# Kernel optimization log

Hardware: AMD Instinct MI355X
Metric: run time of the kernel (lower is better)

## Reference

```python
import jax, jax.numpy as jnp
import numpy as np

B, C, HW, S, G = 256, 512, 16, 256, 32
EPS = 1e-5


def setup_inputs() -> dict:
    key = jax.random.key(0)
    ks = jax.random.split(key, 6)
    scale = 0.02
    return {
        "x": jax.random.normal(ks[0], (B, C, HW, HW), dtype=jnp.float32),
        "gn_w": jnp.ones((C,), dtype=jnp.float32),
        "gn_b": jnp.zeros((C,), dtype=jnp.float32),
        "wq": jax.random.normal(ks[1], (C, C), dtype=jnp.float32) * scale,
        "bq": jnp.zeros((C,), dtype=jnp.float32),
        "wk": jax.random.normal(ks[2], (C, C), dtype=jnp.float32) * scale,
        "bk": jnp.zeros((C,), dtype=jnp.float32),
        "wv": jax.random.normal(ks[3], (C, C), dtype=jnp.float32) * scale,
        "bv": jnp.zeros((C,), dtype=jnp.float32),
        "wp": jax.random.normal(ks[4], (C, C), dtype=jnp.float32) * scale,
        "bp": jnp.zeros((C,), dtype=jnp.float32),
    }


def reference(x, gn_w, gn_b, wq, bq, wk, bk, wv, bv, wp, bp):
    b = x.shape[0]
    # GroupNorm(32, 512): normalize over (channels-in-group, H, W)
    xg = x.reshape(b, G, C // G, HW, HW)
    mu = jnp.mean(xg, axis=(2, 3, 4), keepdims=True)
    var = jnp.var(xg, axis=(2, 3, 4), keepdims=True)
    h = ((xg - mu) * jax.lax.rsqrt(var + EPS)).reshape(b, C, HW, HW)
    h = h * gn_w[:, None, None] + gn_b[:, None, None]
    hf = h.reshape(b, C, S)  # [B, C, S] with S = H*W = 256
    # 1x1 convs == per-pixel linear projections
    q = jnp.einsum('oc,bcs->bos', wq, hf) + bq[:, None]
    k = jnp.einsum('oc,bcs->bos', wk, hf) + bk[:, None]
    v = jnp.einsum('oc,bcs->bos', wv, hf) + bv[:, None]
    # w[b,s,t] = sum_c q[b,c,s] k[b,c,t]; scaled by sqrt(C)=sqrt(512) per source
    att = jnp.einsum('bcs,bct->bst', q, k) / jnp.sqrt(jnp.float32(C))
    att = jax.nn.softmax(att, axis=2)
    # torch: bmm(v, att.permute(0,2,1)) -> out[b,c,t] = sum_s v[b,c,s] att[b,t,s]
    o = jnp.einsum('bcs,bts->bct', v, att)
    o = o.reshape(b, C, HW, HW)
    o = jnp.einsum('oc,bchw->bohw', wp, o) + bp[None, :, None, None]
    return x + o
```

## Files before the change

### kernel.cpp

```cpp
#include <hip/hip_runtime.h>

typedef __attribute__((ext_vector_type(8))) short short8;
typedef __attribute__((ext_vector_type(8))) unsigned short us8;
typedef __attribute__((ext_vector_type(4))) unsigned short us4;
typedef __attribute__((ext_vector_type(4))) float f32x4;

static __device__ __forceinline__ unsigned short f2bf(float f) {
  union { float f; unsigned u; } c; c.f = f;
  unsigned r = (c.u + 0x7FFFu + ((c.u >> 16) & 1u)) >> 16;
  return (unsigned short)r;
}
static __device__ __forceinline__ float b2f(unsigned short h) {
  union { unsigned u; float f; } c; c.u = ((unsigned)h) << 16; return c.f;
}

static __device__ __forceinline__ void gll16(const unsigned short* g, unsigned short* l) {
  __builtin_amdgcn_global_load_lds(
      (const __attribute__((address_space(1))) unsigned int*)g,
      (__attribute__((address_space(3))) unsigned int*)l, 16, 0, 0);
}

__global__ __launch_bounds__(256) void conv_k(
    const float* __restrict__ wv, const float* __restrict__ wp,
    unsigned short* __restrict__ wvb, unsigned short* __restrict__ wpb)
{
  int i4 = (blockIdx.x * 256 + threadIdx.x) * 4;
  const float* src;
  unsigned short* dst;
  if (i4 < 262144) { src = wv + i4; dst = wvb + i4; }
  else             { src = wp + (i4 - 262144); dst = wpb + (i4 - 262144); }
  f32x4 v = *(const f32x4*)src;
  us4 o;
  #pragma unroll
  for (int j = 0; j < 4; ++j) o[j] = f2bf(v[j]);
  *(us4*)dst = o;
}

__global__ __launch_bounds__(256) void tk(
    const float* __restrict__ wq, const float* __restrict__ wk,
    unsigned short* __restrict__ wqT, unsigned short* __restrict__ wkT)
{
  __shared__ float L[64][65];
  const float* src = blockIdx.z ? wk : wq;
  unsigned short* dst = blockIdx.z ? wkT : wqT;
  const int ro = blockIdx.x * 64, co = blockIdx.y * 64;
  const int tid = threadIdx.x;
  #pragma unroll
  for (int p = 0; p < 4; ++p) {
    int lin = p * 1024 + tid * 4;
    int r = lin >> 6, cl = lin & 63;
    *(f32x4*)&L[r][cl] = *(const f32x4*)(src + (size_t)(ro + r) * 512 + co + cl);
  }
  __syncthreads();
  #pragma unroll
  for (int p = 0; p < 4; ++p) {
    int lin = p * 1024 + tid * 4;
    int rr = lin >> 6, cc = lin & 63;
    us4 o;
    #pragma unroll
    for (int j = 0; j < 4; ++j) o[j] = f2bf(L[cc + j][rr]);
    *(us4*)(dst + (size_t)(co + rr) * 512 + ro + cc) = o;
  }
}

__global__ __launch_bounds__(256) void w2b_k(
    const unsigned short* __restrict__ wkT, const float* __restrict__ bq,
    float* __restrict__ w2b)
{
  const int wv_ = threadIdx.x >> 6, lane = threadIdx.x & 63;
  for (int i = 0; i < 16; ++i) {
    const int c = blockIdx.x * 64 + i * 4 + wv_;
    us8 kv = *(const us8*)(wkT + (size_t)c * 512 + lane * 8);
    float s = 0.f;
    #pragma unroll
    for (int j = 0; j < 8; ++j) s += b2f(kv[j]) * bq[lane * 8 + j];
    #pragma unroll
    for (int o = 32; o; o >>= 1) s += __shfl_xor(s, o);
    if (lane == 0) w2b[c] = s;
  }
}

__global__ __launch_bounds__(512) void gn_k(
    const float* __restrict__ x, const float* __restrict__ gw,
    const float* __restrict__ gb, unsigned short* __restrict__ hT)
{
  __shared__ unsigned short tile[32][256];
  __shared__ float rs[2][4][2];
  const int b = blockIdx.x >> 4, gp = blockIdx.x & 15;
  const int tid = threadIdx.x;
  const int sub = tid >> 8;
  const int t = tid & 255;
  const int g = gp * 2 + sub;
  const float* xp = x + ((size_t)b * 512 + g * 16) * 256;
  f32x4 vals[4];
  float s = 0.f, s2 = 0.f;
  #pragma unroll
  for (int j = 0; j < 4; ++j) {
    f32x4 v = *(const f32x4*)(xp + j * 1024 + t * 4);
    vals[j] = v;
    s  += v[0] + v[1] + v[2] + v[3];
    s2 += v[0]*v[0] + v[1]*v[1] + v[2]*v[2] + v[3]*v[3];
  }
  #pragma unroll
  for (int o = 32; o; o >>= 1) { s += __shfl_xor(s, o); s2 += __shfl_xor(s2, o); }
  if ((t & 63) == 0) { rs[sub][t >> 6][0] = s; rs[sub][t >> 6][1] = s2; }
  __syncthreads();
  s  = rs[sub][0][0] + rs[sub][1][0] + rs[sub][2][0] + rs[sub][3][0];
  s2 = rs[sub][0][1] + rs[sub][1][1] + rs[sub][2][1] + rs[sub][3][1];
  const float mean = s * (1.f / 4096.f);
  const float var  = s2 * (1.f / 4096.f) - mean * mean;
  const float rstd = rsqrtf(var + 1e-5f);
  #pragma unroll
  for (int j = 0; j < 4; ++j) {
    const int cl = j * 4 + (t >> 6);
    const int c = g * 16 + cl;
    const float sc = gw[c] * rstd;
    const float sh = gb[c] - mean * sc;
    f32x4 v = vals[j];
    us4 o;
    #pragma unroll
    for (int q = 0; q < 4; ++q) o[q] = f2bf(v[q] * sc + sh);
    *(us4*)&tile[sub * 16 + cl][(t & 63) * 4] = o;
  }
  __syncthreads();
  const int srow = tid >> 1, half = tid & 1;
  us8 o0, o1;
  #pragma unroll
  for (int c = 0; c < 8; ++c) o0[c] = tile[half * 16 + c][srow];
  #pragma unroll
  for (int c = 0; c < 8; ++c) o1[c] = tile[half * 16 + 8 + c][srow];
  unsigned short* dst = hT + ((size_t)b * 256 + srow) * 512 + gp * 32 + half * 16;
  *(us8*)dst = o0;
  *(us8*)(dst + 8) = o1;
}

template<int BM, int BN, int MI, int TPB, int NWN, int NTT,
         int BIAS_MODE, bool OUT_F32, bool HAS_RESID, bool NFAST, int SWZ = 0>
__global__ __launch_bounds__(TPB, 2) void gemmp_k(
    const unsigned short* __restrict__ A, long long sAb, int lda,
    const unsigned short* __restrict__ B, long long sBb, int ldb,
    void* __restrict__ Cv, long long sCb, int ldc,
    const float* __restrict__ bias, const float* __restrict__ resid)
{
  constexpr int CA = BM * 8 / TPB;
  constexpr int CB = BN * 8 / TPB;
  __shared__ unsigned short SMEM[2 * BM * 64 + 2 * BN * 64];
  unsigned short* AsBase = SMEM;
  unsigned short* BsBase = SMEM + 2 * BM * 64;
  const int tid = threadIdx.x;
  int bz, bm, bn;
  if (SWZ) {
    const int L = blockIdx.x;
    const int xcd = L & 7, j = (L >> 3) & 7, bhi = L >> 6;
    bz = bhi * 8 + xcd;
    bm = (j >> 1) * BM;
    bn = (j & 1) * BN;
  } else {
    bz = blockIdx.z;
    bm = (NFAST ? blockIdx.y : blockIdx.x) * BM;
    bn = (NFAST ? blockIdx.x : blockIdx.y) * BN;
  }
  const int lane = tid & 63, w = tid >> 6;
  const int wr = w / NWN, wc = w % NWN;
  const int lr = lane & 15, lg = lane >> 4;
  const int csw = lr & 7;
  const int ko0 = (lg ^ csw) * 8;
  const int ko1 = ((4 + lg) ^ csw) * 8;

  const unsigned short* aSrc[CA]; int aOff[CA];
  #pragma unroll
  for (int p = 0; p < CA; ++p) {
    const int id = p * TPB + tid;
    const int row = id >> 3, cc = (id & 7) ^ (row & 7);
    aSrc[p] = A + (size_t)bz * sAb + (size_t)(bm + row) * lda + cc * 8;
    aOff[p] = id * 8;
  }
  const unsigned short* bSrc[CB]; int bOff[CB];
  #pragma unroll
  for (int p = 0; p < CB; ++p) {
    const int id = p * TPB + tid;
    const int row = id >> 3, cc = (id & 7) ^ (row & 7);
    bSrc[p] = B + (size_t)bz * sBb + (size_t)(bn + row) * ldb + cc * 8;
    bOff[p] = id * 8;
  }

  f32x4 acc[MI][4];
  #pragma unroll
  for (int i = 0; i < MI; ++i)
    #pragma unroll
    for (int j = 0; j < 4; ++j) acc[i][j] = (f32x4){0.f, 0.f, 0.f, 0.f};

  #pragma unroll
  for (int p = 0; p < CA; ++p) gll16(aSrc[p], &AsBase[aOff[p]]);
  #pragma unroll
  for (int p = 0; p < CB; ++p) gll16(bSrc[p], &BsBase[bOff[p]]);
  asm volatile("s_waitcnt vmcnt(0)" ::: "memory");
  __builtin_amdgcn_s_barrier();

  #pragma unroll 2
  for (int t = 0; t < NTT; ++t) {
    if (t + 1 < NTT) {
      const int k1 = (t + 1) * 64, sl = (t + 1) & 1;
      #pragma unroll
      for (int p = 0; p < CA; ++p) gll16(aSrc[p] + k1, &AsBase[sl * BM * 64 + aOff[p]]);
      #pragma unroll
      for (int p = 0; p < CB; ++p) gll16(bSrc[p] + k1, &BsBase[sl * BN * 64 + bOff[p]]);
    }
    const unsigned short* At = &AsBase[(t & 1) * BM * 64];
    const unsigned short* Bt = &BsBase[(t & 1) * BN * 64];
    short8 bf[4][2];
    #pragma unroll
    for (int nj = 0; nj < 4; ++nj) {
      bf[nj][0] = *(const short8*)(Bt + (wc * 64 + nj * 16 + lr) * 64 + ko0);
      bf[nj][1] = *(const short8*)(Bt + (wc * 64 + nj * 16 + lr) * 64 + ko1);
    }
    #pragma unroll
    for (int h = 0; h < MI / 4; ++h) {
      short8 af[4][2];
      #pragma unroll
      for (int mi = 0; mi < 4; ++mi) {
        const int rr = wr * (MI * 16) + h * 64 + mi * 16 + lr;
        af[mi][0] = *(const short8*)(At + rr * 64 + ko0);
        af[mi][1] = *(const short8*)(At + rr * 64 + ko1);
      }
      __builtin_amdgcn_s_setprio(1);
      #pragma unroll
      for (int mi = 0; mi < 4; ++mi)
        #pragma unroll
        for (int nj = 0; nj < 4; ++nj) {
          acc[h * 4 + mi][nj] = __builtin_amdgcn_mfma_f32_16x16x32_bf16(af[mi][0], bf[nj][0], acc[h * 4 + mi][nj], 0, 0, 0);
          acc[h * 4 + mi][nj] = __builtin_amdgcn_mfma_f32_16x16x32_bf16(af[mi][1], bf[nj][1], acc[h * 4 + mi][nj], 0, 0, 0);
        }
      __builtin_amdgcn_s_setprio(0);
    }
    if (t + 1 < NTT) {
      asm volatile("s_waitcnt vmcnt(0)" ::: "memory");
      __builtin_amdgcn_s_barrier();
    }
  }

  #pragma unroll
  for (int mi = 0; mi < MI; ++mi) {
    #pragma unroll
    for (int r = 0; r < 4; ++r) {
      const int rowc = bm + wr * (MI * 16) + mi * 16 + lg * 4 + r;
      const float bv_ = (BIAS_MODE == 1) ? bias[rowc] : 0.f;
      #pragma unroll
      for (int ni = 0; ni < 4; ++ni) {
        const int col = bn + wc * 64 + ni * 16 + lr;
        float vv = acc[mi][ni][r] + bv_;
        if (BIAS_MODE == 2) vv += bias[col];
        const size_t idx = (size_t)bz * sCb + (size_t)rowc * ldc + col;
        if (HAS_RESID) vv += resid[idx];
        if (OUT_F32) ((float*)Cv)[idx] = vv;
        else ((unsigned short*)Cv)[idx] = f2bf(vv);
      }
    }
  }
}

__global__ __launch_bounds__(512, 1) void fused_k(
    const unsigned short* __restrict__ A,
    const unsigned short* __restrict__ B,
    const unsigned short* __restrict__ V,
    unsigned short* __restrict__ O)
{
  __shared__ __attribute__((aligned(16))) char SM[147456];
  unsigned short* AsB = (unsigned short*)SM;
  unsigned short* BsB = (unsigned short*)(SM + 65536);
  unsigned short* attL = (unsigned short*)SM;
  unsigned short* vbuf = (unsigned short*)(SM + 131072);
  float* redm = (float*)(SM + 131072);
  float* reds = redm + 1024;

  const int tid = threadIdx.x;
  const int bz = blockIdx.z;
  const int lane = tid & 63, w = tid >> 6;
  const int wr = w >> 2, wc = w & 3;
  const int lr = lane & 15, lg = lane >> 4;
  const int csw = lr & 7;
  const int ko0 = (lg ^ csw) * 8;
  const int ko1 = ((4 + lg) ^ csw) * 8;

  const int rl = tid >> 3;
  const int gc = (tid & 7) ^ (rl & 7);
  const unsigned short* pA = A + (size_t)bz * 131072 + (size_t)rl * 512 + gc * 8;
  const unsigned short* pB = B + (size_t)bz * 131072 + (size_t)rl * 512 + gc * 8;

  auto stageA = [&](int t, int h) {
    const unsigned short* s = pA + (size_t)h * 65536 + t * 64;
    unsigned short* d = AsB + ((2 * t + h) & 3) * 8192 + tid * 8;
    gll16(s, d);
    gll16(s + 32768, d + 4096);
  };
  auto stageB = [&](int t, int h) {
    const unsigned short* s = pB + (size_t)h * 65536 + t * 64;
    unsigned short* d = BsB + ((2 * t + h) & 3) * 8192 + tid * 8;
    gll16(s, d);
    gll16(s + 32768, d + 4096);
  };

  f32x4 acc[8][4];
  #pragma unroll
  for (int i = 0; i < 8; ++i)
    #pragma unroll
    for (int j = 0; j < 4; ++j) acc[i][j] = (f32x4){0.f, 0.f, 0.f, 0.f};

  stageA(0, 0); stageA(0, 1); stageB(0, 0); stageB(0, 1);
  stageB(1, 0); stageA(1, 0); stageA(1, 1);
  asm volatile("s_waitcnt vmcnt(6)" ::: "memory");
  __builtin_amdgcn_s_barrier();

  constexpr int NT = 8;
  for (int t = 0; t < NT; ++t) {
    const unsigned short* sA = AsB + ((2 * t + wr) & 3) * 8192;
    const unsigned short* sB = BsB + ((2 * t + (wc >> 1)) & 3) * 8192;
    const int bc = (wc & 1) * 64;
    short8 af[4][2], bf0[2][2], bf1[2][2];

    #pragma unroll
    for (int mi = 0; mi < 4; ++mi) {
      af[mi][0] = *(const short8*)(sA + (mi * 16 + lr) * 64 + ko0);
      af[mi][1] = *(const short8*)(sA + (mi * 16 + lr) * 64 + ko1);
    }
    #pragma unroll
    for (int nj = 0; nj < 2; ++nj) {
      bf0[nj][0] = *(const short8*)(sB + (bc + nj * 16 + lr) * 64 + ko0);
      bf0[nj][1] = *(const short8*)(sB + (bc + nj * 16 + lr) * 64 + ko1);
    }
    if (t + 1 < NT) stageB(t + 1, 1);
    __builtin_amdgcn_s_barrier();
    __builtin_amdgcn_s_setprio(1);
    #pragma unroll
    for (int mi = 0; mi < 4; ++mi)
      #pragma unroll
      for (int nj = 0; nj < 2; ++nj) {
        acc[mi][nj] = __builtin_amdgcn_mfma_f32_16x16x32_bf16(af[mi][0], bf0[nj][0], acc[mi][nj], 0, 0, 0);
        acc[mi][nj] = __builtin_amdgcn_mfma_f32_16x16x32_bf16(af[mi][1], bf0[nj][1], acc[mi][nj], 0, 0, 0);
      }
    __builtin_amdgcn_s_setprio(0);
    __builtin_amdgcn_s_barrier();

    #pragma unroll
    for (int nj = 0; nj < 2; ++nj) {
      bf1[nj][0] = *(const short8*)(sB + (bc + 32 + nj * 16 + lr) * 64 + ko0);
      bf1[nj][1] = *(const short8*)(sB + (bc + 32 + nj * 16 + lr) * 64 + ko1);
    }
    __builtin_amdgcn_s_barrier();
    __builtin_amdgcn_s_setprio(1);
    #pragma unroll
    for (int mi = 0; mi < 4; ++mi)
      #pragma unroll
      for (int nj = 0; nj < 2; ++nj) {
        acc[mi][2 + nj] = __builtin_amdgcn_mfma_f32_16x16x32_bf16(af[mi][0], bf1[nj][0], acc[mi][2 + nj], 0, 0, 0);
        acc[mi][2 + nj] = __builtin_amdgcn_mfma_f32_16x16x32_bf16(af[mi][1], bf1[nj][1], acc[mi][2 + nj], 0, 0, 0);
      }
    __builtin_amdgcn_s_setprio(0);
    __builtin_amdgcn_s_barrier();

    #pragma unroll
    for (int mi = 0; mi < 4; ++mi) {
      af[mi][0] = *(const short8*)(sA + (64 + mi * 16 + lr) * 64 + ko0);
      af[mi][1] = *(const short8*)(sA + (64 + mi * 16 + lr) * 64 + ko1);
    }
    if (t + 2 < NT) stageB(t + 2, 0);
    __builtin_amdgcn_s_barrier();
    __builtin_amdgcn_s_setprio(1);
    #pragma unroll
    for (int mi = 0; mi < 4; ++mi)
      #pragma unroll
      for (int nj = 0; nj < 2; ++nj) {
        acc[4 + mi][nj] = __builtin_amdgcn_mfma_f32_16x16x32_bf16(af[mi][0], bf0[nj][0], acc[4 + mi][nj], 0, 0, 0);
        acc[4 + mi][nj] = __builtin_amdgcn_mfma_f32_16x16x32_bf16(af[mi][1], bf0[nj][1], acc[4 + mi][nj], 0, 0, 0);
      }
    __builtin_amdgcn_s_setprio(0);
    __builtin_amdgcn_s_barrier();

    if (t + 2 < NT) { stageA(t + 2, 0); stageA(t + 2, 1); }
    __builtin_amdgcn_s_barrier();
    __builtin_amdgcn_s_setprio(1);
    #pragma unroll
    for (int mi = 0; mi < 4; ++mi)
      #pragma unroll
      for (int nj = 0; nj < 2; ++nj) {
        acc[4 + mi][2 + nj] = __builtin_amdgcn_mfma_f32_16x16x32_bf16(af[mi][0], bf1[nj][0], acc[4 + mi][2 + nj], 0, 0, 0);
        acc[4 + mi][2 + nj] = __builtin_amdgcn_mfma_f32_16x16x32_bf16(af[mi][1], bf1[nj][1], acc[4 + mi][2 + nj], 0, 0, 0);
      }
    __builtin_amdgcn_s_setprio(0);
    if (t == NT - 2)      asm volatile("s_waitcnt vmcnt(0)" ::: "memory");
    else if (t < NT - 2)  asm volatile("s_waitcnt vmcnt(6)" ::: "memory");
    __builtin_amdgcn_s_barrier();
  }

  const float SC = 0.044194173824159216f;
  float rmax[8][4];
  #pragma unroll
  for (int mi = 0; mi < 8; ++mi)
    #pragma unroll
    for (int r = 0; r < 4; ++r) {
      float m = fmaxf(fmaxf(acc[mi][0][r], acc[mi][1][r]),
                      fmaxf(acc[mi][2][r], acc[mi][3][r]));
      #pragma unroll
      for (int o = 1; o <= 8; o <<= 1) m = fmaxf(m, __shfl_xor(m, o));
      rmax[mi][r] = m;
    }
  __syncthreads();
  if (lr == 0) {
    #pragma unroll
    for (int mi = 0; mi < 8; ++mi)
      #pragma unroll
      for (int r = 0; r < 4; ++r)
        redm[(wr * 128 + mi * 16 + lg * 4 + r) * 4 + wc] = rmax[mi][r];
  }
  __syncthreads();
  float rsum[8][4];
  #pragma unroll
  for (int mi = 0; mi < 8; ++mi)
    #pragma unroll
    for (int r = 0; r < 4; ++r) {
      const int row = wr * 128 + mi * 16 + lg * 4 + r;
      f32x4 q = *(const f32x4*)&redm[row * 4];
      const float m = fmaxf(fmaxf(q[0], q[1]), fmaxf(q[2], q[3]));
      float s = 0.f;
      #pragma unroll
      for (int ni = 0; ni < 4; ++ni) {
        float e = __expf((acc[mi][ni][r] - m) * SC);
        acc[mi][ni][r] = e;
        s += e;
      }
      #pragma unroll
      for (int o = 1; o <= 8; o <<= 1) s += __shfl_xor(s, o);
      rsum[mi][r] = s;
    }
  if (lr == 0) {
    #pragma unroll
    for (int mi = 0; mi < 8; ++mi)
      #pragma unroll
      for (int r = 0; r < 4; ++r)
        reds[(wr * 128 + mi * 16 + lg * 4 + r) * 4 + wc] = rsum[mi][r];
  }
  __syncthreads();

  #pragma unroll
  for (int mi = 0; mi < 8; ++mi)
    #pragma unroll
    for (int r = 0; r < 4; ++r) {
      const int trow = wr * 128 + mi * 16 + lg * 4 + r;
      f32x4 q = *(const f32x4*)&reds[trow * 4];
      const float inv = 1.f / (q[0] + q[1] + q[2] + q[3]);
      const int t7 = trow & 7;
      #pragma unroll
      for (int ni = 0; ni < 4; ++ni) {
        const int cw = ni * 2 + (lr >> 3);
        const int off = trow * 256 + wc * 64 + ((cw ^ t7) << 3) + (lr & 7);
        attL[off] = f2bf(acc[mi][ni][r] * inv);
      }
    }
  __syncthreads();

  const unsigned short* Vb = V + (size_t)bz * 131072;
  unsigned short* Ob = O + (size_t)bz * 131072;
  const int vrow = tid >> 3;
  const int vgc = (tid & 7) ^ (vrow & 7);
  for (int pass = 0; pass < 4; ++pass) {
    f32x4 po[8][2];
    #pragma unroll
    for (int i = 0; i < 8; ++i)
      #pragma unroll
      for (int j = 0; j < 2; ++j) po[i][j] = (f32x4){0.f, 0.f, 0.f, 0.f};
    for (int kt = 0; kt < 4; ++kt) {
      #pragma unroll
      for (int p = 0; p < 2; ++p) {
        const int id = p * 512 + tid;
        const int rowv = p * 64 + vrow;
        gll16(Vb + (size_t)(pass * 128 + rowv) * 256 + kt * 64 + vgc * 8,
              vbuf + id * 8);
      }
      asm volatile("s_waitcnt vmcnt(0)" ::: "memory");
      __builtin_amdgcn_s_barrier();
      short8 bfv[2][2];
      #pragma unroll
      for (int nj = 0; nj < 2; ++nj) {
        bfv[nj][0] = *(const short8*)(vbuf + (wc * 32 + nj * 16 + lr) * 64 + ko0);
        bfv[nj][1] = *(const short8*)(vbuf + (wc * 32 + nj * 16 + lr) * 64 + ko1);
      }
      __builtin_amdgcn_s_setprio(1);
      #pragma unroll
      for (int mi = 0; mi < 8; ++mi) {
        const int trow = wr * 128 + mi * 16 + lr;
        const int t7 = trow & 7;
        const unsigned short* ap = attL + trow * 256 + kt * 64;
        short8 afv0 = *(const short8*)(ap + ((lg ^ t7) << 3));
        short8 afv1 = *(const short8*)(ap + (((4 + lg) ^ t7) << 3));
        #pragma unroll
        for (int nj = 0; nj < 2; ++nj) {
          po[mi][nj] = __builtin_amdgcn_mfma_f32_16x16x32_bf16(afv0, bfv[nj][0], po[mi][nj], 0, 0, 0);
          po[mi][nj] = __builtin_amdgcn_mfma_f32_16x16x32_bf16(afv1, bfv[nj][1], po[mi][nj], 0, 0, 0);
        }
      }
      __builtin_amdgcn_s_setprio(0);
      __builtin_amdgcn_s_barrier();
    }
    #pragma unroll
    for (int mi = 0; mi < 8; ++mi)
      #pragma unroll
      for (int r = 0; r < 4; ++r) {
        const int trow = wr * 128 + mi * 16 + lg * 4 + r;
        #pragma unroll
        for (int nj = 0; nj < 2; ++nj) {
          const int c = pass * 128 + wc * 32 + nj * 16 + lr;
          Ob[(size_t)trow * 512 + c] = f2bf(po[mi][nj][r]);
        }
      }
  }
}

extern "C" void kernel_launch(void* const* d_in, const int* in_sizes, int n_in,
                              void* d_out, int out_size, void* d_ws, size_t ws_size,
                              hipStream_t stream)
{
  const float* x   = (const float*)d_in[0];
  const float* gnw = (const float*)d_in[1];
  const float* gnb = (const float*)d_in[2];
  const float* wq  = (const float*)d_in[3];
  const float* bq  = (const float*)d_in[4];
  const float* wk  = (const float*)d_in[5];
  const float* wv  = (const float*)d_in[7];
  const float* bv  = (const float*)d_in[8];
  const float* wp  = (const float*)d_in[9];
  const float* bp  = (const float*)d_in[10];
  float* out = (float*)d_out;

  char* ws = (char*)d_ws;
  unsigned short* W2T   = (unsigned short*)(ws);
  unsigned short* wvb   = (unsigned short*)(ws + 524288);
  unsigned short* wpb   = (unsigned short*)(ws + 1048576);
  unsigned short* wqT   = (unsigned short*)(ws + 1572864);
  unsigned short* wkT   = (unsigned short*)(ws + 2097152);
  float*          w2b   = (float*)(ws + 2621440);
  unsigned short* hT    = (unsigned short*)(ws + 2885632);
  unsigned short* T1    = (unsigned short*)(ws + 69994496ull);
  unsigned short* v     = (unsigned short*)(ws + 137103360ull);
  unsigned short* oT    = hT;

  conv_k<<<512, 256, 0, stream>>>(wv, wp, wvb, wpb);
  tk<<<dim3(8, 8, 2), 256, 0, stream>>>(wq, wk, wqT, wkT);
  w2b_k<<<8, 256, 0, stream>>>(wkT, bq, w2b);
  gemmp_k<128, 128, 4, 256, 2, 8, 0, false, false, false><<<dim3(4, 4, 1), 256, 0, stream>>>(
      wkT, 0, 512, wqT, 0, 512, W2T, 0, 512, nullptr, nullptr);
  gn_k<<<4096, 512, 0, stream>>>(x, gnw, gnb, hT);
  gemmp_k<256, 256, 8, 512, 4, 8, 2, false, false, true><<<dim3(2, 256, 1), 512, 0, stream>>>(
      hT, 0, 512, W2T, 0, 512, T1, 0, 512, w2b, nullptr);
  gemmp_k<128, 128, 4, 256, 2, 8, 1, false, false, false, 1><<<dim3(2048, 1, 1), 256, 0, stream>>>(
      wvb, 0, 512, hT, 131072, 512, v, 131072, 256, bv, nullptr);
  fused_k<<<dim3(1, 1, 256), 512, 0, stream>>>(T1, hT, v, oT);
  gemmp_k<128, 128, 4, 256, 2, 8, 1, true, true, false, 1><<<dim3(2048, 1, 1), 256, 0, stream>>>(
      wpb, 0, 512, oT, 131072, 512, out, 131072, 256, bp, x);
}
```

Before: 300.5 us.

## Single-buffer weight tile in V/proj GEMMs and register-prefetch V in fused attention

```diff
diff --git a/kernel.cpp b/kernel.cpp
--- a/kernel.cpp
+++ b/kernel.cpp
@@ -135,8 +135,9 @@
 }
 
 template<int BM, int BN, int MI, int TPB, int NWN, int NTT,
-         int BIAS_MODE, bool OUT_F32, bool HAS_RESID, bool NFAST, int SWZ = 0>
-__global__ __launch_bounds__(TPB, 2) void gemmp_k(
+         int BIAS_MODE, bool OUT_F32, bool HAS_RESID, bool NFAST,
+         int SWZ = 0, bool SBA = false, int MINW = 2>
+__global__ __launch_bounds__(TPB, MINW) void gemmp_k(
     const unsigned short* __restrict__ A, long long sAb, int lda,
     const unsigned short* __restrict__ B, long long sBb, int ldb,
     void* __restrict__ Cv, long long sCb, int ldc,
@@ -144,9 +145,10 @@
 {
   constexpr int CA = BM * 8 / TPB;
   constexpr int CB = BN * 8 / TPB;
-  __shared__ unsigned short SMEM[2 * BM * 64 + 2 * BN * 64];
+  constexpr int ASL = SBA ? BM * 64 : 2 * BM * 64;
+  __shared__ unsigned short SMEM[ASL + 2 * BN * 64];
   unsigned short* AsBase = SMEM;
-  unsigned short* BsBase = SMEM + 2 * BM * 64;
+  unsigned short* BsBase = SMEM + ASL;
   const int tid = threadIdx.x;
   int bz, bm, bn;
   if (SWZ) {
@@ -201,12 +203,14 @@
   for (int t = 0; t < NTT; ++t) {
     if (t + 1 < NTT) {
       const int k1 = (t + 1) * 64, sl = (t + 1) & 1;
-      #pragma unroll
-      for (int p = 0; p < CA; ++p) gll16(aSrc[p] + k1, &AsBase[sl * BM * 64 + aOff[p]]);
+      if (!SBA) {
+        #pragma unroll
+        for (int p = 0; p < CA; ++p) gll16(aSrc[p] + k1, &AsBase[sl * BM * 64 + aOff[p]]);
+      }
       #pragma unroll
       for (int p = 0; p < CB; ++p) gll16(bSrc[p] + k1, &BsBase[sl * BN * 64 + bOff[p]]);
     }
-    const unsigned short* At = &AsBase[(t & 1) * BM * 64];
+    const unsigned short* At = SBA ? AsBase : &AsBase[(t & 1) * BM * 64];
     const unsigned short* Bt = &BsBase[(t & 1) * BN * 64];
     short8 bf[4][2];
     #pragma unroll
@@ -236,6 +240,13 @@
     if (t + 1 < NTT) {
       asm volatile("s_waitcnt vmcnt(0)" ::: "memory");
       __builtin_amdgcn_s_barrier();
+      if (SBA) {
+        const int k1 = (t + 1) * 64;
+        #pragma unroll
+        for (int p = 0; p < CA; ++p) gll16(aSrc[p] + k1, &AsBase[aOff[p]]);
+        asm volatile("s_waitcnt vmcnt(0)" ::: "memory");
+        __builtin_amdgcn_s_barrier();
+      }
     }
   }
 
@@ -462,6 +473,19 @@
   unsigned short* Ob = O + (size_t)bz * 131072;
   const int vrow = tid >> 3;
   const int vgc = (tid & 7) ^ (vrow & 7);
+  us8 nv0, nv1;
+  auto ldV = [&](int idx) {
+    const int ps = idx >> 2, kt = idx & 3;
+    const unsigned short* s0 = Vb + (size_t)(ps * 128 + vrow) * 256 + kt * 64 + vgc * 8;
+    nv0 = *(const us8*)s0;
+    nv1 = *(const us8*)(s0 + (size_t)64 * 256);
+  };
+  auto stV = [&]() {
+    *(us8*)(vbuf + tid * 8) = nv0;
+    *(us8*)(vbuf + (512 + tid) * 8) = nv1;
+  };
+  ldV(0); stV();
+  __syncthreads();
   for (int pass = 0; pass < 4; ++pass) {
     f32x4 po[8][2];
     #pragma unroll
@@ -469,15 +493,8 @@
       #pragma unroll
       for (int j = 0; j < 2; ++j) po[i][j] = (f32x4){0.f, 0.f, 0.f, 0.f};
     for (int kt = 0; kt < 4; ++kt) {
-      #pragma unroll
-      for (int p = 0; p < 2; ++p) {
-        const int id = p * 512 + tid;
-        const int rowv = p * 64 + vrow;
-        gll16(Vb + (size_t)(pass * 128 + rowv) * 256 + kt * 64 + vgc * 8,
-              vbuf + id * 8);
-      }
-      asm volatile("s_waitcnt vmcnt(0)" ::: "memory");
-      __builtin_amdgcn_s_barrier();
+      const int idx = pass * 4 + kt;
+      if (idx + 1 < 16) ldV(idx + 1);
       short8 bfv[2][2];
       #pragma unroll
       for (int nj = 0; nj < 2; ++nj) {
@@ -499,7 +516,9 @@
         }
       }
       __builtin_amdgcn_s_setprio(0);
-      __builtin_amdgcn_s_barrier();
+      __syncthreads();
+      if (idx + 1 < 16) stV();
+      __syncthreads();
     }
     #pragma unroll
     for (int mi = 0; mi < 8; ++mi)
@@ -551,9 +570,9 @@
   gn_k<<<4096, 512, 0, stream>>>(x, gnw, gnb, hT);
   gemmp_k<256, 256, 8, 512, 4, 8, 2, false, false, true><<<dim3(2, 256, 1), 512, 0, stream>>>(
       hT, 0, 512, W2T, 0, 512, T1, 0, 512, w2b, nullptr);
-  gemmp_k<128, 128, 4, 256, 2, 8, 1, false, false, false, 1><<<dim3(2048, 1, 1), 256, 0, stream>>>(
+  gemmp_k<128, 128, 4, 256, 2, 8, 1, false, false, false, 1, true, 3><<<dim3(2048, 1, 1), 256, 0, stream>>>(
       wvb, 0, 512, hT, 131072, 512, v, 131072, 256, bv, nullptr);
   fused_k<<<dim3(1, 1, 256), 512, 0, stream>>>(T1, hT, v, oT);
-  gemmp_k<128, 128, 4, 256, 2, 8, 1, true, true, false, 1><<<dim3(2048, 1, 1), 256, 0, stream>>>(
+  gemmp_k<128, 128, 4, 256, 2, 8, 1, true, true, false, 1, true, 3><<<dim3(2048, 1, 1), 256, 0, stream>>>(
       wpb, 0, 512, oT, 131072, 512, out, 131072, 256, bp, x);
 }
```

Result: no change. 300.5 us (-0.0%).
